# Optimization experiments

Measured on AMD Instinct MI355X. Metric: run time of the kernel, lower is better.

Reference implementation:

```python
import jax, jax.numpy as jnp
import numpy as np

N = 50000   # num_embs = num nodes
E = 800000  # num edges
D = 256     # feature dim
L = 4       # num layers
EPS = 1e-5


def setup_inputs() -> dict:
    key = jax.random.key(0)
    ks = jax.random.split(key, 8)
    scale = 1.0 / np.sqrt(D)
    return {
        "x": jax.random.normal(ks[0], (N, D), dtype=jnp.float32),  # ignored by forward
        "edge_index": jax.random.randint(ks[1], (2, E), 0, N, dtype=jnp.int32),
        "edge_weight": jax.random.uniform(ks[2], (E,), dtype=jnp.float32),
        "emb_weight": jax.random.normal(ks[3], (N, D), dtype=jnp.float32),
        "ln_w": jnp.ones((L, D), dtype=jnp.float32),
        "ln_b": jnp.zeros((L, D), dtype=jnp.float32),
        "conv_w": jax.random.normal(ks[4], (L, D, D), dtype=jnp.float32) * scale,
        "conv_b": jnp.zeros((L, D), dtype=jnp.float32),
        "post_w": jax.random.normal(ks[5], (D, D), dtype=jnp.float32) * scale,
        "post_b": jnp.zeros((D,), dtype=jnp.float32),
    }


def _layer_norm(h, w, b):
    mu = jnp.mean(h, axis=-1, keepdims=True)
    var = jnp.mean(jnp.square(h - mu), axis=-1, keepdims=True)
    return (h - mu) * jax.lax.rsqrt(var + EPS) * w + b


def reference(x, edge_index, edge_weight, emb_weight, ln_w, ln_b, conv_w, conv_b, post_w, post_b):
    # GCNConv semantics (PyG defaults): add self-loops (weight 1), symmetric norm.
    loop = jnp.arange(N, dtype=edge_index.dtype)
    src = jnp.concatenate([edge_index[0], loop])
    dst = jnp.concatenate([edge_index[1], loop])
    w = jnp.concatenate([edge_weight, jnp.ones((N,), edge_weight.dtype)])
    deg = jax.ops.segment_sum(w, dst, num_segments=N)
    dinv = jnp.where(deg > 0, jax.lax.rsqrt(jnp.maximum(deg, 1e-12)), 0.0)
    coef = (dinv[src] * w * dinv[dst])[:, None]  # [E+N, 1]

    h = emb_weight  # forward ignores x; cond_emb is None
    for i in range(L):
        z = _layer_norm(h, ln_w[i], ln_b[i])          # node LayerNorm
        zw = z @ conv_w[i]                             # linear transform
        agg = jax.ops.segment_sum(coef * zw[src], dst, num_segments=N)
        z = agg + conv_b[i]
        z = jax.nn.gelu(z, approximate=False)          # torch GELU is exact
        h = z + h                                      # residual (dropout=0)
    return h @ post_w + post_b
```

## Files before the change

### kernel.cpp

```cpp
#include <hip/hip_runtime.h>
#include <hip/hip_bf16.h>

#define N_NODES 50000
#define N_EDGES 800000
#define DIM     256
#define NLAYERS 4
#define EPS     1e-5f
#define SCAN_B  196
#define MASK40  ((1ULL << 40) - 1)
#define EPACK_CAP (N_EDGES + 15 * N_NODES + 32)
#define ASTRIDE 258

typedef __bf16 bf16x8 __attribute__((ext_vector_type(8)));
typedef float  f32x4  __attribute__((ext_vector_type(4)));
typedef float  f32x2  __attribute__((ext_vector_type(2)));
typedef unsigned short u16x8 __attribute__((ext_vector_type(8)));
typedef unsigned short u16x4 __attribute__((ext_vector_type(4)));
typedef int            i32x4 __attribute__((ext_vector_type(4)));
typedef unsigned int   u32x2 __attribute__((ext_vector_type(2)));

__device__ __forceinline__ unsigned short f2b(float f) {
    __hip_bfloat16 h = __float2bfloat16(f);
    return __builtin_bit_cast(unsigned short, h);
}
__device__ __forceinline__ float b2f(unsigned short u) {
    unsigned int v = ((unsigned int)u) << 16;
    return __builtin_bit_cast(float, v);
}
__device__ __forceinline__ float gelu_exact(float x) {
    float ax = fabsf(x) * 0.70710678118654752f;
    float t  = 1.0f / (1.0f + 0.3275911f * ax);
    float p  = t * (0.254829592f + t * (-0.284496736f +
               t * (1.421413741f + t * (-1.453152027f + t * 1.061405429f))));
    float er = 1.0f - p * __expf(-ax * ax);
    er = (x < 0.0f) ? -er : er;
    return 0.5f * x * (1.0f + er);
}
__device__ __forceinline__ unsigned int pack_fp8x4(float a, float b, float c, float d) {
    int v = 0;
    v = __builtin_amdgcn_cvt_pk_fp8_f32(a, b, v, false);
    v = __builtin_amdgcn_cvt_pk_fp8_f32(c, d, v, true);
    return (unsigned int)v;
}

__global__ __launch_bounds__(256) void hist_kernel(const int* __restrict__ dst,
                                                   const float* __restrict__ w,
                                                   unsigned long long* __restrict__ cnt64,
                                                   int* __restrict__ rank) {
    int e = blockIdx.x * 256 + threadIdx.x;
    if (e >= N_EDGES) return;
    int d = dst[e];
    unsigned long long wfix = (unsigned long long)(w[e] * 4294967296.0f);
    unsigned long long old = atomicAdd(&cnt64[d], (1ULL << 40) | wfix);
    rank[e] = (int)(old >> 40);
}

__global__ __launch_bounds__(256) void scan_a_kernel(const unsigned long long* __restrict__ cnt64,
                                                     float* __restrict__ dinv,
                                                     int* __restrict__ bsum) {
    __shared__ int l[256];
    int i = blockIdx.x * 256 + threadIdx.x;
    int pc = 0;
    if (i < N_NODES) {
        unsigned long long v = cnt64[i];
        int cnt = (int)(v >> 40);
        float sw = (float)(v & MASK40) * 2.3283064365386963e-10f;
        dinv[i] = rsqrtf(1.0f + sw);
        pc = (cnt + 15) & ~15;
    }
    l[threadIdx.x] = pc;
    __syncthreads();
    for (int o = 128; o > 0; o >>= 1) {
        if (threadIdx.x < o) l[threadIdx.x] += l[threadIdx.x + o];
        __syncthreads();
    }
    if (threadIdx.x == 0) bsum[blockIdx.x] = l[0];
}

__global__ __launch_bounds__(256) void scan_b_kernel(const int* __restrict__ bsum,
                                                     int* __restrict__ boff,
                                                     int* __restrict__ rowptr) {
    __shared__ int l[256];
    int t = threadIdx.x;
    l[t] = (t < SCAN_B) ? bsum[t] : 0;
    __syncthreads();
    if (t == 0) {
        int run = 0;
        for (int j = 0; j < SCAN_B; ++j) { int v = l[j]; l[j] = run; run += v; }
        rowptr[N_NODES] = run;
    }
    __syncthreads();
    boff[t] = l[t];
}

__global__ __launch_bounds__(256) void scan_c_kernel(const unsigned long long* __restrict__ cnt64,
                                                     const int* __restrict__ boff,
                                                     int* __restrict__ rowptr) {
    __shared__ int l[256];
    int i = blockIdx.x * 256 + threadIdx.x;
    int pc = 0;
    if (i < N_NODES) {
        int cnt = (int)(cnt64[i] >> 40);
        pc = (cnt + 15) & ~15;
    }
    l[threadIdx.x] = pc;
    __syncthreads();
    if (threadIdx.x == 0) {
        int run = 0;
        for (int j = 0; j < 256; ++j) { int v = l[j]; l[j] = run; run += v; }
    }
    __syncthreads();
    if (i < N_NODES) rowptr[i] = boff[blockIdx.x] + l[threadIdx.x];
}

__global__ __launch_bounds__(256) void fill_kernel(const int* __restrict__ src,
                                                   const int* __restrict__ dst,
                                                   const float* __restrict__ w,
                                                   const float* __restrict__ dinv,
                                                   const int* __restrict__ rowptr,
                                                   const int* __restrict__ rank,
                                                   int2* __restrict__ epack) {
    int e = blockIdx.x * 256 + threadIdx.x;
    if (e >= N_EDGES) return;
    int s = src[e], d = dst[e];
    float c = dinv[s] * w[e] * dinv[d];
    int p = rowptr[d] + rank[e];
    epack[p] = make_int2(s << 8, __float_as_int(c));
}

__global__ __launch_bounds__(256) void convw_kernel(const float* __restrict__ conv_w,
                                                    const float* __restrict__ post_w,
                                                    unsigned short* __restrict__ Wt) {
    int idx = blockIdx.x * 256 + threadIdx.x;
    if (idx >= 5 * 65536) return;
    int m  = idx >> 16;
    int r  = idx & 65535;
    int ks = r >> 13;
    int n  = (r >> 5) & 255;
    int ke = r & 31;
    int k  = ks * 32 + ke;
    float v = (m < 4) ? conv_w[m * 65536 + k * 256 + n] : post_w[k * 256 + n];
    Wt[idx] = f2b(v);
}

__global__ __launch_bounds__(256) void ln_cast_kernel(const float* __restrict__ H,
                                                      const float* __restrict__ lnw,
                                                      const float* __restrict__ lnb,
                                                      unsigned char* __restrict__ Z8,
                                                      unsigned short* __restrict__ Hbf) {
    int row = blockIdx.x * 4 + (threadIdx.x >> 6);
    int lane = threadIdx.x & 63;
    const float4 x = *(const float4*)(H + (size_t)row * DIM + lane * 4);
    float s = x.x + x.y + x.z + x.w;
    for (int o = 32; o > 0; o >>= 1) s += __shfl_xor(s, o);
    float mu = s * (1.0f / DIM);
    float d0 = x.x - mu, d1 = x.y - mu, d2 = x.z - mu, d3 = x.w - mu;
    float v = d0 * d0 + d1 * d1 + d2 * d2 + d3 * d3;
    for (int o = 32; o > 0; o >>= 1) v += __shfl_xor(v, o);
    float rs = rsqrtf(v * (1.0f / DIM) + EPS);
    const float4 ww = *(const float4*)(lnw + lane * 4);
    const float4 bb = *(const float4*)(lnb + lane * 4);
    float z0 = d0 * rs * ww.x + bb.x;
    float z1 = d1 * rs * ww.y + bb.y;
    float z2 = d2 * rs * ww.z + bb.z;
    float z3 = d3 * rs * ww.w + bb.w;
    *(unsigned int*)(Z8 + (size_t)row * DIM + lane * 4) = pack_fp8x4(z0, z1, z2, z3);
    ushort4 h4;
    h4.x = f2b(x.x); h4.y = f2b(x.y); h4.z = f2b(x.z); h4.w = f2b(x.w);
    *(ushort4*)(Hbf + (size_t)row * DIM + lane * 4) = h4;
}

__global__ __launch_bounds__(256, 4) void layer_kernel(const unsigned char* __restrict__ Z8in,
                                                       const int* __restrict__ rowptr,
                                                       const int2* __restrict__ epack,
                                                       const float* __restrict__ dinv,
                                                       const unsigned short* __restrict__ Bt,
                                                       const float* __restrict__ bias,
                                                       unsigned short* __restrict__ Hbf,
                                                       const float* __restrict__ lnw,
                                                       const float* __restrict__ lnb,
                                                       unsigned char* __restrict__ Z8out,
                                                       int doLN) {
    __shared__ unsigned short atile[32 * ASTRIDE];
    int tid = threadIdx.x;
    int wave = tid >> 6;
    int lane = tid & 63;
    int q = lane >> 4;
    int c16 = lane & 15;
    int g = lane >> 5;
    int colB = (lane & 31) * 8;
    int mbase = blockIdx.x * 32;
    int cbase = wave * 64;

    for (int i = 0; i < 8; ++i) {
        int nl = wave * 8 + i;
        int node = mbase + nl;
        f32x2 a0 = {0.f, 0.f}, a1 = a0, a2 = a0, a3 = a0;
        if (node < N_NODES) {
            float di = dinv[node];
            float scg = (g == 0) ? di * di : 0.0f;
            const u32x2 zs = *(const u32x2*)(Z8in + (size_t)node * DIM + colB);
            {
                f32x2 p0 = __builtin_amdgcn_cvt_pk_f32_fp8(zs[0], false);
                f32x2 p1 = __builtin_amdgcn_cvt_pk_f32_fp8(zs[0], true);
                f32x2 p2 = __builtin_amdgcn_cvt_pk_f32_fp8(zs[1], false);
                f32x2 p3 = __builtin_amdgcn_cvt_pk_f32_fp8(zs[1], true);
                a0 = scg * p0; a1 = scg * p1; a2 = scg * p2; a3 = scg * p3;
            }
            int e0 = rowptr[node], e1 = rowptr[node + 1];
            for (int e = e0; e < e1; e += 16) {
                const int2* pp = epack + e + 8 * g;
                const i32x4 q0 = *(const i32x4*)pp;
                const i32x4 q1 = *(const i32x4*)(pp + 2);
                const i32x4 q2 = *(const i32x4*)(pp + 4);
                const i32x4 q3 = *(const i32x4*)(pp + 6);
                const u32x2 v0 = *(const u32x2*)(Z8in + q0[0] + colB);
                const u32x2 v1 = *(const u32x2*)(Z8in + q0[2] + colB);
                const u32x2 v2 = *(const u32x2*)(Z8in + q1[0] + colB);
                const u32x2 v3 = *(const u32x2*)(Z8in + q1[2] + colB);
                const u32x2 v4 = *(const u32x2*)(Z8in + q2[0] + colB);
                const u32x2 v5 = *(const u32x2*)(Z8in + q2[2] + colB);
                const u32x2 v6 = *(const u32x2*)(Z8in + q3[0] + colB);
                const u32x2 v7 = *(const u32x2*)(Z8in + q3[2] + colB);
                float c0 = __int_as_float(q0[1]), c1 = __int_as_float(q0[3]);
                float c2 = __int_as_float(q1[1]), c3 = __int_as_float(q1[3]);
                float c4 = __int_as_float(q2[1]), c5 = __int_as_float(q2[3]);
                float c6 = __int_as_float(q3[1]), c7 = __int_as_float(q3[3]);
                #pragma unroll
                for (int h = 0; h < 8; ++h) {
                    u32x2 vv; float cc;
                    switch (h) {
                        case 0: vv = v0; cc = c0; break;
                        case 1: vv = v1; cc = c1; break;
                        case 2: vv = v2; cc = c2; break;
                        case 3: vv = v3; cc = c3; break;
                        case 4: vv = v4; cc = c4; break;
                        case 5: vv = v5; cc = c5; break;
                        case 6: vv = v6; cc = c6; break;
                        default: vv = v7; cc = c7; break;
                    }
                    f32x2 p0 = __builtin_amdgcn_cvt_pk_f32_fp8(vv[0], false);
                    f32x2 p1 = __builtin_amdgcn_cvt_pk_f32_fp8(vv[0], true);
                    f32x2 p2 = __builtin_amdgcn_cvt_pk_f32_fp8(vv[1], false);
                    f32x2 p3 = __builtin_amdgcn_cvt_pk_f32_fp8(vv[1], true);
                    a0 += cc * p0; a1 += cc * p1; a2 += cc * p2; a3 += cc * p3;
                }
            }
        }
        float a[8] = {a0[0], a0[1], a1[0], a1[1], a2[0], a2[1], a3[0], a3[1]};
        #pragma unroll
        for (int j = 0; j < 8; ++j) a[j] += __shfl_xor(a[j], 32);
        if (g == 0) {
            u16x8 z;
            #pragma unroll
            for (int j = 0; j < 8; ++j) z[j] = f2b(a[j]);
            *(u16x8*)&atile[nl * ASTRIDE + colB] = z;
        }
    }
    __syncthreads();

    int aoffL[2];
    #pragma unroll
    for (int nt = 0; nt < 2; ++nt)
        aoffL[nt] = (nt * 16 + c16) * ASTRIDE + q * 8;
    int woff[4];
    #pragma unroll
    for (int ct = 0; ct < 4; ++ct)
        woff[ct] = (cbase + ct * 16 + c16) * 32 + q * 8;

    f32x4 acc[2][4] = {};
    #pragma unroll
    for (int ks = 0; ks < 8; ++ks) {
        bf16x8 nf[2], wf[4];
        #pragma unroll
        for (int nt = 0; nt < 2; ++nt)
            nf[nt] = __builtin_bit_cast(bf16x8, *(const u16x8*)&atile[aoffL[nt] + ks * 32]);
        #pragma unroll
        for (int ct = 0; ct < 4; ++ct)
            wf[ct] = __builtin_bit_cast(bf16x8, *(const u16x8*)(Bt + ks * 8192 + woff[ct]));
        #pragma unroll
        for (int nt = 0; nt < 2; ++nt)
            #pragma unroll
            for (int ct = 0; ct < 4; ++ct)
                acc[nt][ct] = __builtin_amdgcn_mfma_f32_16x16x32_bf16(wf[ct], nf[nt], acc[nt][ct], 0, 0, 0);
    }
    __syncthreads();

    #pragma unroll
    for (int nt = 0; nt < 2; ++nt) {
        int row = nt * 16 + c16;
        #pragma unroll
        for (int ct = 0; ct < 4; ++ct) {
            int col = cbase + ct * 16 + q * 4;
            u16x4 pk;
            pk[0] = f2b(acc[nt][ct][0]);
            pk[1] = f2b(acc[nt][ct][1]);
            pk[2] = f2b(acc[nt][ct][2]);
            pk[3] = f2b(acc[nt][ct][3]);
            *(u16x4*)&atile[row * ASTRIDE + col] = pk;
        }
    }
    __syncthreads();

    int r  = tid >> 3;
    int cb = (tid & 7) * 32;
    int node = mbase + r;
    if (node < N_NODES) {
        float h[32];
        float psum = 0.0f, psq = 0.0f;
        #pragma unroll
        for (int i = 0; i < 4; ++i) {
            const u16x8 sv = *(const u16x8*)&atile[r * ASTRIDE + cb + i * 8];
            const f32x4 b0 = *(const f32x4*)(bias + cb + i * 8);
            const f32x4 b1 = *(const f32x4*)(bias + cb + i * 8 + 4);
            const u16x8 hv = *(const u16x8*)(Hbf + (size_t)node * DIM + cb + i * 8);
            #pragma unroll
            for (int j = 0; j < 8; ++j) {
                float v = b2f(sv[j]) + (j < 4 ? b0[j] : b1[j - 4]);
                float hn = gelu_exact(v) + b2f(hv[j]);
                h[i * 8 + j] = hn;
                psum += hn;
                psq += hn * hn;
            }
        }
        #pragma unroll
        for (int i = 0; i < 4; ++i) {
            u16x8 hw;
            #pragma unroll
            for (int j = 0; j < 8; ++j) hw[j] = f2b(h[i * 8 + j]);
            *(u16x8*)(Hbf + (size_t)node * DIM + cb + i * 8) = hw;
        }
        if (doLN) {
            psum += __shfl_xor(psum, 1);
            psum += __shfl_xor(psum, 2);
            psum += __shfl_xor(psum, 4);
            psq  += __shfl_xor(psq, 1);
            psq  += __shfl_xor(psq, 2);
            psq  += __shfl_xor(psq, 4);
            float mu = psum * (1.0f / DIM);
            float var = fmaxf(psq * (1.0f / DIM) - mu * mu, 0.0f);
            float rs = rsqrtf(var + EPS);
            #pragma unroll
            for (int i2 = 0; i2 < 2; ++i2) {
                int c0 = cb + i2 * 16;
                unsigned int pk[4];
                #pragma unroll
                for (int k = 0; k < 4; ++k) {
                    const f32x4 ww = *(const f32x4*)(lnw + c0 + k * 4);
                    const f32x4 lb = *(const f32x4*)(lnb + c0 + k * 4);
                    int hb = i2 * 16 + k * 4;
                    float y0 = (h[hb + 0] - mu) * rs * ww[0] + lb[0];
                    float y1 = (h[hb + 1] - mu) * rs * ww[1] + lb[1];
                    float y2 = (h[hb + 2] - mu) * rs * ww[2] + lb[2];
                    float y3 = (h[hb + 3] - mu) * rs * ww[3] + lb[3];
                    pk[k] = pack_fp8x4(y0, y1, y2, y3);
                }
                uint4 st = make_uint4(pk[0], pk[1], pk[2], pk[3]);
                *(uint4*)(Z8out + (size_t)node * DIM + c0) = st;
            }
        }
    }
}

__global__ __launch_bounds__(256, 4) void gemm_out_kernel(const unsigned short* __restrict__ A,
                                                          const unsigned short* __restrict__ Bt,
                                                          float* __restrict__ C,
                                                          const float* __restrict__ bias) {
    int tid = threadIdx.x;
    int wave = tid >> 6;
    int lane = tid & 63;
    int q = lane >> 4;
    int c16 = lane & 15;
    int mbase = blockIdx.x * 32;
    int cbase = wave * 64;

    const unsigned short* aptr[2];
    #pragma unroll
    for (int nt = 0; nt < 2; ++nt) {
        int row = mbase + nt * 16 + c16;
        if (row >= N_NODES) row = N_NODES - 1;
        aptr[nt] = A + (size_t)row * DIM + q * 8;
    }
    int woff[4];
    #pragma unroll
    for (int ct = 0; ct < 4; ++ct)
        woff[ct] = (cbase + ct * 16 + c16) * 32 + q * 8;

    f32x4 acc[2][4] = {};
    #pragma unroll
    for (int ks = 0; ks < 8; ++ks) {
        bf16x8 nf[2], wf[4];
        #pragma unroll
        for (int nt = 0; nt < 2; ++nt)
            nf[nt] = __builtin_bit_cast(bf16x8, *(const u16x8*)(aptr[nt] + ks * 32));
        #pragma unroll
        for (int ct = 0; ct < 4; ++ct)
            wf[ct] = __builtin_bit_cast(bf16x8, *(const u16x8*)(Bt + ks * 8192 + woff[ct]));
        #pragma unroll
        for (int nt = 0; nt < 2; ++nt)
            #pragma unroll
            for (int ct = 0; ct < 4; ++ct)
                acc[nt][ct] = __builtin_amdgcn_mfma_f32_16x16x32_bf16(nf[nt], wf[ct], acc[nt][ct], 0, 0, 0);
    }

    float bb[4];
    #pragma unroll
    for (int ct = 0; ct < 4; ++ct)
        bb[ct] = bias[cbase + ct * 16 + c16];
    #pragma unroll
    for (int nt = 0; nt < 2; ++nt) {
        #pragma unroll
        for (int j = 0; j < 4; ++j) {
            int node = mbase + nt * 16 + q * 4 + j;
            if (node >= N_NODES) continue;
            #pragma unroll
            for (int ct = 0; ct < 4; ++ct) {
                int chan = cbase + ct * 16 + c16;
                C[(size_t)node * DIM + chan] = acc[nt][ct][j] + bb[ct];
            }
        }
    }
}

extern "C" void kernel_launch(void* const* d_in, const int* in_sizes, int n_in,
                              void* d_out, int out_size, void* d_ws, size_t ws_size,
                              hipStream_t stream) {
    const int*   ei     = (const int*)d_in[1];
    const int*   src    = ei;
    const int*   dst    = ei + N_EDGES;
    const float* ew     = (const float*)d_in[2];
    const float* emb    = (const float*)d_in[3];
    const float* ln_w   = (const float*)d_in[4];
    const float* ln_b   = (const float*)d_in[5];
    const float* conv_w = (const float*)d_in[6];
    const float* conv_b = (const float*)d_in[7];
    const float* post_w = (const float*)d_in[8];
    const float* post_b = (const float*)d_in[9];
    float* out = (float*)d_out;

    char* w = (char*)d_ws;
    size_t off = 0;
    auto alloc = [&](size_t bytes) -> char* {
        char* p = w + off;
        off += (bytes + 255) & ~(size_t)255;
        return p;
    };
    unsigned long long* cnt64 = (unsigned long long*)alloc((size_t)N_NODES * 8);
    float* dinv   = (float*)alloc((size_t)N_NODES * 4);
    int*   rank   = (int*)alloc((size_t)N_EDGES * 4);
    int*   rowptr = (int*)alloc((size_t)(N_NODES + 1) * 4);
    int*   bsum   = (int*)alloc(256 * 4);
    int*   boff   = (int*)alloc(256 * 4);
    int2*  epack  = (int2*)alloc((size_t)EPACK_CAP * 8);
    unsigned short* Wt  = (unsigned short*)alloc((size_t)5 * 65536 * 2);
    unsigned char*  Z8a = (unsigned char*)alloc((size_t)N_NODES * DIM);
    unsigned char*  Z8b = (unsigned char*)alloc((size_t)N_NODES * DIM);
    unsigned short* Hbf = (unsigned short*)alloc((size_t)N_NODES * DIM * 2);

    hipMemsetAsync(cnt64, 0, (size_t)N_NODES * 8, stream);
    hipMemsetAsync(epack, 0, (size_t)EPACK_CAP * 8, stream);
    hist_kernel<<<N_EDGES / 256, 256, 0, stream>>>(dst, ew, cnt64, rank);
    scan_a_kernel<<<SCAN_B, 256, 0, stream>>>(cnt64, dinv, bsum);
    scan_b_kernel<<<1, 256, 0, stream>>>(bsum, boff, rowptr);
    scan_c_kernel<<<SCAN_B, 256, 0, stream>>>(cnt64, boff, rowptr);
    fill_kernel<<<N_EDGES / 256, 256, 0, stream>>>(src, dst, ew, dinv, rowptr, rank, epack);
    convw_kernel<<<(5 * 65536) / 256, 256, 0, stream>>>(conv_w, post_w, Wt);

    const int GRID = (N_NODES + 31) / 32;
    ln_cast_kernel<<<N_NODES / 4, 256, 0, stream>>>(emb, ln_w, ln_b, Z8a, Hbf);
    for (int l = 0; l < NLAYERS; ++l) {
        const unsigned char* zin  = (l & 1) ? Z8b : Z8a;
        unsigned char*       zout = (l & 1) ? Z8a : Z8b;
        int doLN = (l < NLAYERS - 1) ? 1 : 0;
        const float* nlw = doLN ? (ln_w + (l + 1) * DIM) : ln_w;
        const float* nlb = doLN ? (ln_b + (l + 1) * DIM) : ln_b;
        layer_kernel<<<GRID, 256, 0, stream>>>(zin, rowptr, epack, dinv,
                                               Wt + (size_t)l * 65536,
                                               conv_b + (size_t)l * DIM, Hbf,
                                               nlw, nlb, zout, doLN);
    }
    gemm_out_kernel<<<GRID, 256, 0, stream>>>(Hbf, Wt + (size_t)4 * 65536, out, post_b);
}
```

Baseline: 564.3 us.

## Warp-specialize layer kernel into gather producer and MFMA consumer waves with double buffering

The layer kernel becomes a persistent grid of 512 blocks with 384 threads. Four waves gather the neighbour aggregation for the next 32-node tile into a double-buffered shared tile, while two consumer waves run the bf16 MFMA transform, GELU, residual and next-layer LayerNorm on the current tile. The aim is to overlap memory-bound gathering with the matmul and epilogue instead of running them in sequence inside each block. In exchange, each consumer wave does 16x8 MFMAs per tile and re-reads the weights from global memory, so the consumer side may become the bottleneck. Shared memory use doubles, which can lower occupancy.

After: 1.420 ms. 152% more time.

```diff
diff --git a/kernel.cpp b/kernel.cpp
--- a/kernel.cpp
+++ b/kernel.cpp
@@ -10,6 +10,9 @@
 #define MASK40  ((1ULL << 40) - 1)
 #define EPACK_CAP (N_EDGES + 15 * N_NODES + 32)
 #define ASTRIDE 258
+#define SSTRIDE 258
+#define NTILES  1563
+#define GRIDB   512
 
 typedef __bf16 bf16x8 __attribute__((ext_vector_type(8)));
 typedef float  f32x4  __attribute__((ext_vector_type(4)));
@@ -170,7 +173,7 @@
     *(ushort4*)(Hbf + (size_t)row * DIM + lane * 4) = h4;
 }
 
-__global__ __launch_bounds__(256, 4) void layer_kernel(const unsigned char* __restrict__ Z8in,
+__global__ __launch_bounds__(384, 4) void layer_kernel(const unsigned char* __restrict__ Z8in,
                                                        const int* __restrict__ rowptr,
                                                        const int2* __restrict__ epack,
                                                        const float* __restrict__ dinv,
@@ -181,7 +184,8 @@
                                                        const float* __restrict__ lnb,
                                                        unsigned char* __restrict__ Z8out,
                                                        int doLN) {
-    __shared__ unsigned short atile[32 * ASTRIDE];
+    __shared__ unsigned short abuf[2][32 * ASTRIDE];
+    __shared__ unsigned short stripe[2][16 * SSTRIDE];
     int tid = threadIdx.x;
     int wave = tid >> 6;
     int lane = tid & 63;
@@ -189,176 +193,182 @@
     int c16 = lane & 15;
     int g = lane >> 5;
     int colB = (lane & 31) * 8;
-    int mbase = blockIdx.x * 32;
-    int cbase = wave * 64;
-
-    for (int i = 0; i < 8; ++i) {
-        int nl = wave * 8 + i;
-        int node = mbase + nl;
-        f32x2 a0 = {0.f, 0.f}, a1 = a0, a2 = a0, a3 = a0;
-        if (node < N_NODES) {
-            float di = dinv[node];
-            float scg = (g == 0) ? di * di : 0.0f;
-            const u32x2 zs = *(const u32x2*)(Z8in + (size_t)node * DIM + colB);
-            {
-                f32x2 p0 = __builtin_amdgcn_cvt_pk_f32_fp8(zs[0], false);
-                f32x2 p1 = __builtin_amdgcn_cvt_pk_f32_fp8(zs[0], true);
-                f32x2 p2 = __builtin_amdgcn_cvt_pk_f32_fp8(zs[1], false);
-                f32x2 p3 = __builtin_amdgcn_cvt_pk_f32_fp8(zs[1], true);
-                a0 = scg * p0; a1 = scg * p1; a2 = scg * p2; a3 = scg * p3;
-            }
-            int e0 = rowptr[node], e1 = rowptr[node + 1];
-            for (int e = e0; e < e1; e += 16) {
-                const int2* pp = epack + e + 8 * g;
-                const i32x4 q0 = *(const i32x4*)pp;
-                const i32x4 q1 = *(const i32x4*)(pp + 2);
-                const i32x4 q2 = *(const i32x4*)(pp + 4);
-                const i32x4 q3 = *(const i32x4*)(pp + 6);
-                const u32x2 v0 = *(const u32x2*)(Z8in + q0[0] + colB);
-                const u32x2 v1 = *(const u32x2*)(Z8in + q0[2] + colB);
-                const u32x2 v2 = *(const u32x2*)(Z8in + q1[0] + colB);
-                const u32x2 v3 = *(const u32x2*)(Z8in + q1[2] + colB);
-                const u32x2 v4 = *(const u32x2*)(Z8in + q2[0] + colB);
-                const u32x2 v5 = *(const u32x2*)(Z8in + q2[2] + colB);
-                const u32x2 v6 = *(const u32x2*)(Z8in + q3[0] + colB);
-                const u32x2 v7 = *(const u32x2*)(Z8in + q3[2] + colB);
-                float c0 = __int_as_float(q0[1]), c1 = __int_as_float(q0[3]);
-                float c2 = __int_as_float(q1[1]), c3 = __int_as_float(q1[3]);
-                float c4 = __int_as_float(q2[1]), c5 = __int_as_float(q2[3]);
-                float c6 = __int_as_float(q3[1]), c7 = __int_as_float(q3[3]);
+
+    int nt = (NTILES - blockIdx.x + GRIDB - 1) / GRIDB;
+
+    auto gather_tile = [&](int tile, int buf) {
+        int mbase = tile * 32;
+        for (int i = 0; i < 8; ++i) {
+            int nl = wave * 8 + i;
+            int node = mbase + nl;
+            f32x2 a0 = {0.f, 0.f}, a1 = a0, a2 = a0, a3 = a0;
+            if (node < N_NODES) {
+                float di = dinv[node];
+                float scg = (g == 0) ? di * di : 0.0f;
+                const u32x2 zs = *(const u32x2*)(Z8in + (size_t)node * DIM + colB);
+                {
+                    f32x2 p0 = __builtin_amdgcn_cvt_pk_f32_fp8(zs[0], false);
+                    f32x2 p1 = __builtin_amdgcn_cvt_pk_f32_fp8(zs[0], true);
+                    f32x2 p2 = __builtin_amdgcn_cvt_pk_f32_fp8(zs[1], false);
+                    f32x2 p3 = __builtin_amdgcn_cvt_pk_f32_fp8(zs[1], true);
+                    a0 = scg * p0; a1 = scg * p1; a2 = scg * p2; a3 = scg * p3;
+                }
+                int e0 = rowptr[node], e1 = rowptr[node + 1];
+                for (int e = e0; e < e1; e += 16) {
+                    const int2* pp = epack + e + 8 * g;
+                    const i32x4 q0 = *(const i32x4*)pp;
+                    const i32x4 q1 = *(const i32x4*)(pp + 2);
+                    const i32x4 q2 = *(const i32x4*)(pp + 4);
+                    const i32x4 q3 = *(const i32x4*)(pp + 6);
+                    const u32x2 v0 = *(const u32x2*)(Z8in + q0[0] + colB);
+                    const u32x2 v1 = *(const u32x2*)(Z8in + q0[2] + colB);
+                    const u32x2 v2 = *(const u32x2*)(Z8in + q1[0] + colB);
+                    const u32x2 v3 = *(const u32x2*)(Z8in + q1[2] + colB);
+                    const u32x2 v4 = *(const u32x2*)(Z8in + q2[0] + colB);
+                    const u32x2 v5 = *(const u32x2*)(Z8in + q2[2] + colB);
+                    const u32x2 v6 = *(const u32x2*)(Z8in + q3[0] + colB);
+                    const u32x2 v7 = *(const u32x2*)(Z8in + q3[2] + colB);
+                    float c0 = __int_as_float(q0[1]), c1 = __int_as_float(q0[3]);
+                    float c2 = __int_as_float(q1[1]), c3 = __int_as_float(q1[3]);
+                    float c4 = __int_as_float(q2[1]), c5 = __int_as_float(q2[3]);
+                    float c6 = __int_as_float(q3[1]), c7 = __int_as_float(q3[3]);
+                    #pragma unroll
+                    for (int h = 0; h < 8; ++h) {
+                        u32x2 vv; float cc;
+                        switch (h) {
+                            case 0: vv = v0; cc = c0; break;
+                            case 1: vv = v1; cc = c1; break;
+                            case 2: vv = v2; cc = c2; break;
+                            case 3: vv = v3; cc = c3; break;
+                            case 4: vv = v4; cc = c4; break;
+                            case 5: vv = v5; cc = c5; break;
+                            case 6: vv = v6; cc = c6; break;
+                            default: vv = v7; cc = c7; break;
+                        }
+                        f32x2 p0 = __builtin_amdgcn_cvt_pk_f32_fp8(vv[0], false);
+                        f32x2 p1 = __builtin_amdgcn_cvt_pk_f32_fp8(vv[0], true);
+                        f32x2 p2 = __builtin_amdgcn_cvt_pk_f32_fp8(vv[1], false);
+                        f32x2 p3 = __builtin_amdgcn_cvt_pk_f32_fp8(vv[1], true);
+                        a0 += cc * p0; a1 += cc * p1; a2 += cc * p2; a3 += cc * p3;
+                    }
+                }
+            }
+            float a[8] = {a0[0], a0[1], a1[0], a1[1], a2[0], a2[1], a3[0], a3[1]};
+            #pragma unroll
+            for (int j = 0; j < 8; ++j) a[j] += __shfl_xor(a[j], 32);
+            if (g == 0) {
+                u16x8 z;
                 #pragma unroll
-                for (int h = 0; h < 8; ++h) {
-                    u32x2 vv; float cc;
-                    switch (h) {
-                        case 0: vv = v0; cc = c0; break;
-                        case 1: vv = v1; cc = c1; break;
-                        case 2: vv = v2; cc = c2; break;
-                        case 3: vv = v3; cc = c3; break;
-                        case 4: vv = v4; cc = c4; break;
-                        case 5: vv = v5; cc = c5; break;
-                        case 6: vv = v6; cc = c6; break;
-                        default: vv = v7; cc = c7; break;
-                    }
-                    f32x2 p0 = __builtin_amdgcn_cvt_pk_f32_fp8(vv[0], false);
-                    f32x2 p1 = __builtin_amdgcn_cvt_pk_f32_fp8(vv[0], true);
-                    f32x2 p2 = __builtin_amdgcn_cvt_pk_f32_fp8(vv[1], false);
-                    f32x2 p3 = __builtin_amdgcn_cvt_pk_f32_fp8(vv[1], true);
-                    a0 += cc * p0; a1 += cc * p1; a2 += cc * p2; a3 += cc * p3;
-                }
-            }
-        }
-        float a[8] = {a0[0], a0[1], a1[0], a1[1], a2[0], a2[1], a3[0], a3[1]};
-        #pragma unroll
-        for (int j = 0; j < 8; ++j) a[j] += __shfl_xor(a[j], 32);
-        if (g == 0) {
-            u16x8 z;
-            #pragma unroll
-            for (int j = 0; j < 8; ++j) z[j] = f2b(a[j]);
-            *(u16x8*)&atile[nl * ASTRIDE + colB] = z;
-        }
-    }
-    __syncthreads();
-
-    int aoffL[2];
-    #pragma unroll
-    for (int nt = 0; nt < 2; ++nt)
-        aoffL[nt] = (nt * 16 + c16) * ASTRIDE + q * 8;
-    int woff[4];
-    #pragma unroll
-    for (int ct = 0; ct < 4; ++ct)
-        woff[ct] = (cbase + ct * 16 + c16) * 32 + q * 8;
-
-    f32x4 acc[2][4] = {};
-    #pragma unroll
-    for (int ks = 0; ks < 8; ++ks) {
-        bf16x8 nf[2], wf[4];
-        #pragma unroll
-        for (int nt = 0; nt < 2; ++nt)
-            nf[nt] = __builtin_bit_cast(bf16x8, *(const u16x8*)&atile[aoffL[nt] + ks * 32]);
-        #pragma unroll
-        for (int ct = 0; ct < 4; ++ct)
-            wf[ct] = __builtin_bit_cast(bf16x8, *(const u16x8*)(Bt + ks * 8192 + woff[ct]));
-        #pragma unroll
-        for (int nt = 0; nt < 2; ++nt)
-            #pragma unroll
-            for (int ct = 0; ct < 4; ++ct)
-                acc[nt][ct] = __builtin_amdgcn_mfma_f32_16x16x32_bf16(wf[ct], nf[nt], acc[nt][ct], 0, 0, 0);
-    }
-    __syncthreads();
-
-    #pragma unroll
-    for (int nt = 0; nt < 2; ++nt) {
-        int row = nt * 16 + c16;
-        #pragma unroll
-        for (int ct = 0; ct < 4; ++ct) {
-            int col = cbase + ct * 16 + q * 4;
+                for (int j = 0; j < 8; ++j) z[j] = f2b(a[j]);
+                *(u16x8*)&abuf[buf][nl * ASTRIDE + colB] = z;
+            }
+        }
+    };
+
+    auto consume_tile = [&](int tile, int buf) {
+        int c = wave - 4;
+        int mbase = tile * 32;
+        int nodeRow = c * 16 + c16;
+
+        bf16x8 nf[8];
+        #pragma unroll
+        for (int ks = 0; ks < 8; ++ks)
+            nf[ks] = __builtin_bit_cast(bf16x8,
+                *(const u16x8*)&abuf[buf][nodeRow * ASTRIDE + ks * 32 + q * 8]);
+
+        f32x4 acc[16];
+        #pragma unroll
+        for (int ct = 0; ct < 16; ++ct) {
+            acc[ct] = f32x4{0.f, 0.f, 0.f, 0.f};
+            int woff = (ct * 16 + c16) * 32 + q * 8;
+            #pragma unroll
+            for (int ks = 0; ks < 8; ++ks) {
+                bf16x8 wf = __builtin_bit_cast(bf16x8,
+                    *(const u16x8*)(Bt + ks * 8192 + woff));
+                acc[ct] = __builtin_amdgcn_mfma_f32_16x16x32_bf16(wf, nf[ks], acc[ct], 0, 0, 0);
+            }
+        }
+
+        #pragma unroll
+        for (int ct = 0; ct < 16; ++ct) {
             u16x4 pk;
-            pk[0] = f2b(acc[nt][ct][0]);
-            pk[1] = f2b(acc[nt][ct][1]);
-            pk[2] = f2b(acc[nt][ct][2]);
-            pk[3] = f2b(acc[nt][ct][3]);
-            *(u16x4*)&atile[row * ASTRIDE + col] = pk;
-        }
-    }
-    __syncthreads();
-
-    int r  = tid >> 3;
-    int cb = (tid & 7) * 32;
-    int node = mbase + r;
-    if (node < N_NODES) {
-        float h[32];
+            pk[0] = f2b(acc[ct][0]);
+            pk[1] = f2b(acc[ct][1]);
+            pk[2] = f2b(acc[ct][2]);
+            pk[3] = f2b(acc[ct][3]);
+            *(u16x4*)&stripe[c][c16 * SSTRIDE + ct * 16 + q * 4] = pk;
+        }
+
+        int r  = lane >> 2;
+        int ck = lane & 3;
+        int node = mbase + c * 16 + r;
+        if (node >= N_NODES) return;
+        int cb = ck * 64;
         float psum = 0.0f, psq = 0.0f;
         #pragma unroll
-        for (int i = 0; i < 4; ++i) {
-            const u16x8 sv = *(const u16x8*)&atile[r * ASTRIDE + cb + i * 8];
+        for (int i = 0; i < 8; ++i) {
+            const u16x8 sv = *(const u16x8*)&stripe[c][r * SSTRIDE + cb + i * 8];
             const f32x4 b0 = *(const f32x4*)(bias + cb + i * 8);
             const f32x4 b1 = *(const f32x4*)(bias + cb + i * 8 + 4);
             const u16x8 hv = *(const u16x8*)(Hbf + (size_t)node * DIM + cb + i * 8);
+            u16x8 hw;
             #pragma unroll
             for (int j = 0; j < 8; ++j) {
                 float v = b2f(sv[j]) + (j < 4 ? b0[j] : b1[j - 4]);
                 float hn = gelu_exact(v) + b2f(hv[j]);
-                h[i * 8 + j] = hn;
+                hw[j] = f2b(hn);
                 psum += hn;
                 psq += hn * hn;
             }
-        }
-        #pragma unroll
-        for (int i = 0; i < 4; ++i) {
-            u16x8 hw;
-            #pragma unroll
-            for (int j = 0; j < 8; ++j) hw[j] = f2b(h[i * 8 + j]);
             *(u16x8*)(Hbf + (size_t)node * DIM + cb + i * 8) = hw;
-        }
-        if (doLN) {
-            psum += __shfl_xor(psum, 1);
-            psum += __shfl_xor(psum, 2);
-            psum += __shfl_xor(psum, 4);
-            psq  += __shfl_xor(psq, 1);
-            psq  += __shfl_xor(psq, 2);
-            psq  += __shfl_xor(psq, 4);
-            float mu = psum * (1.0f / DIM);
-            float var = fmaxf(psq * (1.0f / DIM) - mu * mu, 0.0f);
-            float rs = rsqrtf(var + EPS);
-            #pragma unroll
-            for (int i2 = 0; i2 < 2; ++i2) {
-                int c0 = cb + i2 * 16;
-                unsigned int pk[4];
-                #pragma unroll
-                for (int k = 0; k < 4; ++k) {
-                    const f32x4 ww = *(const f32x4*)(lnw + c0 + k * 4);
-                    const f32x4 lb = *(const f32x4*)(lnb + c0 + k * 4);
-                    int hb = i2 * 16 + k * 4;
-                    float y0 = (h[hb + 0] - mu) * rs * ww[0] + lb[0];
-                    float y1 = (h[hb + 1] - mu) * rs * ww[1] + lb[1];
-                    float y2 = (h[hb + 2] - mu) * rs * ww[2] + lb[2];
-                    float y3 = (h[hb + 3] - mu) * rs * ww[3] + lb[3];
-                    pk[k] = pack_fp8x4(y0, y1, y2, y3);
+            *(u16x8*)&stripe[c][r * SSTRIDE + cb + i * 8] = hw;
+        }
+        if (!doLN) return;
+        psum += __shfl_xor(psum, 1);
+        psum += __shfl_xor(psum, 2);
+        psq  += __shfl_xor(psq, 1);
+        psq  += __shfl_xor(psq, 2);
+        float mu = psum * (1.0f / DIM);
+        float var = fmaxf(psq * (1.0f / DIM) - mu * mu, 0.0f);
+        float rs = rsqrtf(var + EPS);
+        #pragma unroll
+        for (int i2 = 0; i2 < 4; ++i2) {
+            int c0 = cb + i2 * 16;
+            const u16x8 h0 = *(const u16x8*)&stripe[c][r * SSTRIDE + c0];
+            const u16x8 h1 = *(const u16x8*)&stripe[c][r * SSTRIDE + c0 + 8];
+            unsigned int pk[4];
+            #pragma unroll
+            for (int k = 0; k < 4; ++k) {
+                const f32x4 ww = *(const f32x4*)(lnw + c0 + k * 4);
+                const f32x4 lb = *(const f32x4*)(lnb + c0 + k * 4);
+                float y0, y1, y2, y3;
+                if (k < 2) {
+                    y0 = (b2f(h0[k * 4 + 0]) - mu) * rs * ww[0] + lb[0];
+                    y1 = (b2f(h0[k * 4 + 1]) - mu) * rs * ww[1] + lb[1];
+                    y2 = (b2f(h0[k * 4 + 2]) - mu) * rs * ww[2] + lb[2];
+                    y3 = (b2f(h0[k * 4 + 3]) - mu) * rs * ww[3] + lb[3];
+                } else {
+                    y0 = (b2f(h1[(k - 2) * 4 + 0]) - mu) * rs * ww[0] + lb[0];
+                    y1 = (b2f(h1[(k - 2) * 4 + 1]) - mu) * rs * ww[1] + lb[1];
+                    y2 = (b2f(h1[(k - 2) * 4 + 2]) - mu) * rs * ww[2] + lb[2];
+                    y3 = (b2f(h1[(k - 2) * 4 + 3]) - mu) * rs * ww[3] + lb[3];
                 }
-                uint4 st = make_uint4(pk[0], pk[1], pk[2], pk[3]);
-                *(uint4*)(Z8out + (size_t)node * DIM + c0) = st;
-            }
-        }
+                pk[k] = pack_fp8x4(y0, y1, y2, y3);
+            }
+            uint4 st = make_uint4(pk[0], pk[1], pk[2], pk[3]);
+            *(uint4*)(Z8out + (size_t)node * DIM + c0) = st;
+        }
+    };
+
+    if (wave < 4) gather_tile(blockIdx.x, 0);
+    __syncthreads();
+    for (int it = 0; it < nt; ++it) {
+        if (wave < 4) {
+            if (it + 1 < nt) gather_tile(blockIdx.x + (it + 1) * GRIDB, (it + 1) & 1);
+        } else {
+            consume_tile(blockIdx.x + it * GRIDB, it & 1);
+        }
+        __syncthreads();
     }
 }
 
@@ -466,7 +476,6 @@
     fill_kernel<<<N_EDGES / 256, 256, 0, stream>>>(src, dst, ew, dinv, rowptr, rank, epack);
     convw_kernel<<<(5 * 65536) / 256, 256, 0, stream>>>(conv_w, post_w, Wt);
 
-    const int GRID = (N_NODES + 31) / 32;
     ln_cast_kernel<<<N_NODES / 4, 256, 0, stream>>>(emb, ln_w, ln_b, Z8a, Hbf);
     for (int l = 0; l < NLAYERS; ++l) {
         const unsigned char* zin  = (l & 1) ? Z8b : Z8a;
@@ -474,10 +483,10 @@
         int doLN = (l < NLAYERS - 1) ? 1 : 0;
         const float* nlw = doLN ? (ln_w + (l + 1) * DIM) : ln_w;
         const float* nlb = doLN ? (ln_b + (l + 1) * DIM) : ln_b;
-        layer_kernel<<<GRID, 256, 0, stream>>>(zin, rowptr, epack, dinv,
-                                               Wt + (size_t)l * 65536,
-                                               conv_b + (size_t)l * DIM, Hbf,
-                                               nlw, nlb, zout, doLN);
-    }
-    gemm_out_kernel<<<GRID, 256, 0, stream>>>(Hbf, Wt + (size_t)4 * 65536, out, post_b);
-}
+        layer_kernel<<<GRIDB, 384, 0, stream>>>(zin, rowptr, epack, dinv,
+                                                Wt + (size_t)l * 65536,
+                                                conv_b + (size_t)l * DIM, Hbf,
+                                                nlw, nlb, zout, doLN);
+    }
+    gemm_out_kernel<<<(N_NODES + 31) / 32, 256, 0, stream>>>(Hbf, Wt + (size_t)4 * 65536, out, post_b);
+}
```
